# Performance work log

Measured on AMD Instinct MI355X. Metric: run time of the kernel, lower is better.

The kernel has to match this reference:

```python
import jax, jax.numpy as jnp
import numpy as np

B, Q, C = 8, 100, 1024
H, W = 64, 64
NH = 16
HD = C // NH
SCALE = HD ** -0.5
LN_EPS = 1e-5


def setup_inputs() -> dict:
    key = jax.random.key(0)
    ks = jax.random.split(key, 8)
    xav = lambda k, shp: jax.random.normal(k, shp, jnp.float32) * (2.0 / (shp[0] + shp[-1])) ** 0.5
    return {
        "tgt": jax.random.normal(ks[0], (B, Q, C), jnp.float32),
        "memory": jax.random.normal(ks[1], (B, H, W, C), jnp.float32),
        "memory_pos_emb": jax.random.normal(ks[2], (B, H, W, C), jnp.float32),
        "query_pos_emb": jax.random.normal(ks[3], (B, Q, C), jnp.float32),
        "Wq": xav(ks[4], (C, C)),
        "Wk": xav(ks[5], (C, C)),
        "Wv": xav(ks[6], (C, C)),
        "Wo": xav(ks[7], (C, C)),
        "bo": jnp.zeros((C,), jnp.float32),
        "ln_gamma": jnp.ones((C,), jnp.float32),
        "ln_beta": jnp.zeros((C,), jnp.float32),
    }


def _layernorm(x, g, b):
    mu = jnp.mean(x, axis=-1, keepdims=True)
    var = jnp.var(x, axis=-1, keepdims=True)
    return (x - mu) * jax.lax.rsqrt(var + LN_EPS) * g + b


def reference(tgt, memory, memory_pos_emb, query_pos_emb, Wq, Wk, Wv, Wo, bo, ln_gamma, ln_beta):
    # flatten spatial dims: [B,H,W,C] -> [B,K,C]
    mem = memory.reshape(B, H * W, C)
    mpos = memory_pos_emb.reshape(B, H * W, C)
    q_in = tgt + query_pos_emb          # [B,Q,C]
    k_in = mem + mpos                    # [B,K,C]
    # projections (torch Linear: x @ W.T), split heads -> [B,nh,*,hd]
    q = (q_in @ Wq.T).reshape(B, Q, NH, HD).transpose(0, 2, 1, 3)
    k = (k_in @ Wk.T).reshape(B, -1, NH, HD).transpose(0, 2, 1, 3)
    v = (mem @ Wv.T).reshape(B, -1, NH, HD).transpose(0, 2, 1, 3)
    dots = jnp.einsum('bhid,bhjd->bhij', q, k) * SCALE   # [B,nh,Q,K]
    # slot attention: softmax over QUERY axis, then renormalize over keys
    attn = jax.nn.softmax(dots, axis=2)
    attn = attn / (jnp.sum(attn, axis=-1, keepdims=True) + 1e-8)
    updates = jnp.einsum('bhij,bhjd->bhid', attn, v)     # [B,nh,Q,hd]
    updates = updates.transpose(0, 2, 1, 3).reshape(B, Q, C)
    out = updates @ Wo.T + bo
    # residual (dropout is identity in eval) + post-LayerNorm
    return _layernorm(tgt + out, ln_gamma, ln_beta)
```

## Files before the change

### kernel.cpp

```cpp
#include <hip/hip_runtime.h>

typedef unsigned short u16;
typedef __attribute__((ext_vector_type(8))) short bf16x8;
typedef __attribute__((ext_vector_type(4))) short bf16x4;
typedef __attribute__((ext_vector_type(4))) float f32x4;
typedef __attribute__((ext_vector_type(4))) unsigned short u16x4;
typedef __attribute__((ext_vector_type(4))) int i32x4;
typedef __attribute__((ext_vector_type(4))) float f4;

#define DI __device__ __forceinline__


DI u16 f2bf(float f){
  unsigned int u = __float_as_uint(f);
  return (u16)((u + 0x7FFFu + ((u >> 16) & 1u)) >> 16);
}

DI void gl_lds16(const void* g, void* l){
  __builtin_amdgcn_global_load_lds((const __attribute__((address_space(1))) unsigned int*)g,
                                   (__attribute__((address_space(3))) unsigned int*)l, 16, 0, 0);
}

__global__ __launch_bounds__(256) void prep_kv(const float* __restrict__ mem,
                                               const float* __restrict__ mpos,
                                               u16* __restrict__ kA, u16* __restrict__ vA){
  size_t gid = (size_t)blockIdx.x * 256 + threadIdx.x;
  f4 m = ((const f4*)mem)[gid];
  f4 p = ((const f4*)mpos)[gid];
  u16x4 k, v;
  #pragma unroll
  for (int j = 0; j < 4; ++j){ k[j] = f2bf(m[j] + p[j]); v[j] = f2bf(m[j]); }
  ((u16x4*)kA)[gid] = k;
  ((u16x4*)vA)[gid] = v;
}

__global__ __launch_bounds__(256) void prep_qw(const float* __restrict__ tgt,
                                               const float* __restrict__ qpos,
                                               const float* __restrict__ Wq, const float* __restrict__ Wk,
                                               const float* __restrict__ Wv, const float* __restrict__ Wo,
                                               u16* __restrict__ qA, u16* __restrict__ Wbf){
  int gid = blockIdx.x * 256 + threadIdx.x;
  const int NQ4 = 819200 / 4;
  if (gid < NQ4){
    f4 a = ((const f4*)tgt)[gid];
    f4 b = ((const f4*)qpos)[gid];
    u16x4 r;
    #pragma unroll
    for (int j = 0; j < 4; ++j) r[j] = f2bf(a[j] + b[j]);
    ((u16x4*)qA)[gid] = r;
  } else {
    int wid = gid - NQ4;
    int sel = wid >> 18;
    int off = wid & 262143;
    const float* W = (sel == 0) ? Wq : (sel == 1) ? Wk : (sel == 2) ? Wv : Wo;
    f4 w = ((const f4*)W)[off];
    u16x4 r;
    #pragma unroll
    for (int j = 0; j < 4; ++j) r[j] = f2bf(w[j]);
    ((u16x4*)(Wbf))[(size_t)sel * 262144 + off] = r;
  }
}

template<int MODE>
__global__ __launch_bounds__(256, 2) void gemm_bt(
    const u16* __restrict__ A, const u16* __restrict__ Bw,
    u16* __restrict__ Cb, float* __restrict__ Cf,
    const float* __restrict__ bias, const float* __restrict__ resid,
    int M, float scale)
{
  __shared__ u16 lA[2][128 * 32];
  __shared__ u16 lB[2][128 * 32];
  const int tid = threadIdx.x;
  const int l = tid & 63, w = tid >> 6;
  const int nwg = gridDim.x;
  int bid = blockIdx.x;
  bid = (bid & 7) * (nwg >> 3) + (bid >> 3);
  const int mb = bid >> 3, nb = bid & 7;
  const int m0 = mb * 128, n0 = nb * 128;
  const int fr = l & 15, fg = l >> 4;
  const int wr = w >> 1, wc = w & 1;

  f32x4 acc[4][4] = {};

  auto stage = [&](int buf, int kt){
    const int k0 = kt * 32;
    #pragma unroll
    for (int q = 0; q < 2; ++q){
      int r = w * 32 + q * 16 + (l >> 2);
      int ar = m0 + r; if (ar >= M) ar = M - 1;
      gl_lds16(A  + (size_t)ar * 1024 + k0 + (l & 3) * 8, &lA[buf][(w * 32 + q * 16) * 32]);
      gl_lds16(Bw + (size_t)(n0 + r) * 1024 + k0 + (l & 3) * 8, &lB[buf][(w * 32 + q * 16) * 32]);
    }
  };

  stage(0, 0);
  __syncthreads();
  for (int kt = 0; kt < 32; ++kt){
    const int cur = kt & 1;
    if (kt < 31) stage(cur ^ 1, kt + 1);
    bf16x8 av[4], bv[4];
    #pragma unroll
    for (int m = 0; m < 4; ++m)
      av[m] = *(const bf16x8*)&lA[cur][(wr * 64 + m * 16 + fr) * 32 + fg * 8];
    #pragma unroll
    for (int n = 0; n < 4; ++n)
      bv[n] = *(const bf16x8*)&lB[cur][(wc * 64 + n * 16 + fr) * 32 + fg * 8];
    #pragma unroll
    for (int m = 0; m < 4; ++m)
      #pragma unroll
      for (int n = 0; n < 4; ++n)
        acc[m][n] = __builtin_amdgcn_mfma_f32_16x16x32_bf16(av[m], bv[n], acc[m][n], 0, 0, 0);
    __syncthreads();
  }

  #pragma unroll
  for (int m = 0; m < 4; ++m){
    const int grow_base = m0 + wr * 64 + m * 16 + fg * 4;
    #pragma unroll
    for (int n = 0; n < 4; ++n){
      const int gcol = n0 + wc * 64 + n * 16 + fr;
      #pragma unroll
      for (int r = 0; r < 4; ++r){
        const int grow = grow_base + r;
        if (grow < M){
          const float v = acc[m][n][r];
          if (MODE == 0) Cb[(size_t)grow * 1024 + gcol] = f2bf(v * scale);
          else           Cf[(size_t)grow * 1024 + gcol] = v + bias[gcol] + resid[(size_t)grow * 1024 + gcol];
        }
      }
    }
  }
}

__global__ __launch_bounds__(64, 1) void attn_k(
    const u16* __restrict__ qp, const u16* __restrict__ kp, const u16* __restrict__ vp,
    float* __restrict__ updpart, float* __restrict__ rspart)
{
  const int bidx = blockIdx.x;
  const int c = bidx & 7, h = (bidx >> 3) & 15, b = bidx >> 7;
  const int bh = b * 16 + h;
  const int l = threadIdx.x;
  const int fr = l & 15, fg = l >> 4;

  __shared__ u16 qlds[112 * 64];
  for (int t = 0; t < 14; ++t){
    int chunk = t * 64 + l;
    int row = chunk >> 3, cb = chunk & 7;
    i32x4 val = {0, 0, 0, 0};
    if (row < 100)
      val = *(const i32x4*)(qp + (size_t)(b * 100 + row) * 1024 + h * 64 + cb * 8);
    *(i32x4*)((char*)qlds + row * 128 + ((cb ^ (row & 7)) * 16)) = val;
  }
  __syncthreads();

  bf16x8 qf[7][2];
  #pragma unroll
  for (int n = 0; n < 7; ++n)
    #pragma unroll
    for (int ks = 0; ks < 2; ++ks){
      int row = n * 16 + fr;
      int cb = ks * 4 + fg;
      qf[n][ks] = *(const bf16x8*)((const char*)qlds + row * 128 + ((cb ^ (row & 7)) * 16));
    }

  f32x4 acc[7][4] = {};
  float rs[7] = {};
  const f32x4 fz = {0.f, 0.f, 0.f, 0.f};
  const size_t kvbase = ((size_t)b * 4096) * 1024 + h * 64;

  for (int t = 0; t < 32; ++t){
    const int j0 = c * 512 + t * 16;
    bf16x8 kf0 = *(const bf16x8*)(kp + kvbase + (size_t)(j0 + fr) * 1024 + fg * 8);
    bf16x8 kf1 = *(const bf16x8*)(kp + kvbase + (size_t)(j0 + fr) * 1024 + 32 + fg * 8);
    f32x4 s[7];
    #pragma unroll
    for (int n = 0; n < 7; ++n){
      s[n] = __builtin_amdgcn_mfma_f32_16x16x32_bf16(kf0, qf[n][0], fz, 0, 0, 0);
      s[n] = __builtin_amdgcn_mfma_f32_16x16x32_bf16(kf1, qf[n][1], s[n], 0, 0, 0);
    }
    if (fr >= 4){ s[6][0] = -1e30f; s[6][1] = -1e30f; s[6][2] = -1e30f; s[6][3] = -1e30f; }

    float pv[7][4];
    #pragma unroll
    for (int r = 0; r < 4; ++r){
      float m = s[0][r];
      #pragma unroll
      for (int n = 1; n < 7; ++n) m = fmaxf(m, s[n][r]);
      m = fmaxf(m, __shfl_xor(m, 1)); m = fmaxf(m, __shfl_xor(m, 2));
      m = fmaxf(m, __shfl_xor(m, 4)); m = fmaxf(m, __shfl_xor(m, 8));
      float sum = 0.f;
      #pragma unroll
      for (int n = 0; n < 7; ++n){ float e = __expf(s[n][r] - m); pv[n][r] = e; sum += e; }
      sum += __shfl_xor(sum, 1); sum += __shfl_xor(sum, 2);
      sum += __shfl_xor(sum, 4); sum += __shfl_xor(sum, 8);
      float inv = 1.0f / sum;
      #pragma unroll
      for (int n = 0; n < 7; ++n) pv[n][r] *= inv;
    }

    bf16x4 pk[7];
    #pragma unroll
    for (int n = 0; n < 7; ++n){
      rs[n] += pv[n][0] + pv[n][1] + pv[n][2] + pv[n][3];
      bf16x4 t4;
      t4[0] = (short)f2bf(pv[n][0]); t4[1] = (short)f2bf(pv[n][1]);
      t4[2] = (short)f2bf(pv[n][2]); t4[3] = (short)f2bf(pv[n][3]);
      pk[n] = t4;
    }

    bf16x4 vf[4];
    #pragma unroll
    for (int dt = 0; dt < 4; ++dt){
      bf16x4 tv;
      #pragma unroll
      for (int jj = 0; jj < 4; ++jj)
        tv[jj] = (short)vp[kvbase + (size_t)(j0 + fg * 4 + jj) * 1024 + dt * 16 + fr];
      vf[dt] = tv;
    }

    #pragma unroll
    for (int n = 0; n < 7; ++n)
      #pragma unroll
      for (int dt = 0; dt < 4; ++dt)
        acc[n][dt] = __builtin_amdgcn_mfma_f32_16x16x16bf16_1k(vf[dt], pk[n], acc[n][dt], 0, 0, 0);
  }

  #pragma unroll
  for (int n = 0; n < 7; ++n){
    float v = rs[n];
    v += __shfl_xor(v, 16); v += __shfl_xor(v, 32);
    if (l < 16) rspart[((size_t)c * 128 + bh) * 112 + n * 16 + l] = v;
  }
  float* ub = updpart + ((size_t)c * 128 + bh) * 64 * 112;
  #pragma unroll
  for (int n = 0; n < 7; ++n)
    #pragma unroll
    for (int dt = 0; dt < 4; ++dt)
      #pragma unroll
      for (int r = 0; r < 4; ++r){
        int d = dt * 16 + fg * 4 + r;
        int i = n * 16 + fr;
        ub[d * 112 + i] = acc[n][dt][r];
      }
}

__global__ __launch_bounds__(256) void nrm_k(const float* __restrict__ updpart,
                                             const float* __restrict__ rspart,
                                             u16* __restrict__ updn){
  int gid = blockIdx.x * 256 + threadIdx.x;
  int b = gid / 102400;
  int rem = gid % 102400;
  int i = rem / 1024;
  int cc = rem & 1023;
  int h = cc >> 6, d = cc & 63;
  int bh = b * 16 + h;
  float sum = 0.f, rsum = 0.f;
  #pragma unroll
  for (int c = 0; c < 8; ++c){
    sum  += updpart[(((size_t)c * 128 + bh) * 64 + d) * 112 + i];
    rsum += rspart[((size_t)c * 128 + bh) * 112 + i];
  }
  updn[gid] = f2bf(sum / (rsum + 1e-8f));
}

__global__ __launch_bounds__(256) void ln_k(const float* __restrict__ x,
                                            const float* __restrict__ g,
                                            const float* __restrict__ be,
                                            float* __restrict__ out){
  const int row = blockIdx.x;
  const int tid = threadIdx.x;
  const f4 xv = *(const f4*)(x + (size_t)row * 1024 + tid * 4);
  float s = xv[0] + xv[1] + xv[2] + xv[3];
  float q = xv[0]*xv[0] + xv[1]*xv[1] + xv[2]*xv[2] + xv[3]*xv[3];
  #pragma unroll
  for (int m = 1; m < 64; m <<= 1){ s += __shfl_xor(s, m); q += __shfl_xor(q, m); }
  __shared__ float ss[4], qq[4];
  const int w = tid >> 6;
  if ((tid & 63) == 0){ ss[w] = s; qq[w] = q; }
  __syncthreads();
  s = ss[0] + ss[1] + ss[2] + ss[3];
  q = qq[0] + qq[1] + qq[2] + qq[3];
  const float mu = s * (1.0f / 1024.0f);
  const float var = q * (1.0f / 1024.0f) - mu * mu;
  const float rstd = rsqrtf(var + 1e-5f);
  const f4 gv = *(const f4*)(g + tid * 4);
  const f4 bv = *(const f4*)(be + tid * 4);
  f4 o;
  #pragma unroll
  for (int j = 0; j < 4; ++j) o[j] = (xv[j] - mu) * rstd * gv[j] + bv[j];
  *(f4*)(out + (size_t)row * 1024 + tid * 4) = o;
}

extern "C" void kernel_launch(void* const* d_in, const int* in_sizes, int n_in,
                              void* d_out, int out_size, void* d_ws, size_t ws_size,
                              hipStream_t stream)
{
  const float* tgt   = (const float*)d_in[0];
  const float* mem   = (const float*)d_in[1];
  const float* mpos  = (const float*)d_in[2];
  const float* qpos  = (const float*)d_in[3];
  const float* Wq    = (const float*)d_in[4];
  const float* Wk    = (const float*)d_in[5];
  const float* Wv    = (const float*)d_in[6];
  const float* Wo    = (const float*)d_in[7];
  const float* bo    = (const float*)d_in[8];
  const float* gamma = (const float*)d_in[9];
  const float* beta  = (const float*)d_in[10];

  char* ws = (char*)d_ws;
  u16* qA     = (u16*)(ws + 0);
  u16* Wbf    = (u16*)(ws + 1638400);
  u16* kA     = (u16*)(ws + 10027008);
  u16* vA     = (u16*)(ws + 77135872);
  u16* qproj  = (u16*)(ws + 144244736);
  u16* kproj  = (u16*)(ws + 145883136);
  u16* vproj  = kA;
  float* updpart = (float*)(ws + 77135872);
  float* rspart  = (float*)(ws + 77135872 + 29360128);
  u16*   updn    = (u16*)  (ws + 77135872 + 29818880);
  float* resid   = (float*)(ws + 77135872 + 31457280);

  prep_kv<<<32768, 256, 0, stream>>>(mem, mpos, kA, vA);
  prep_qw<<<4896, 256, 0, stream>>>(tgt, qpos, Wq, Wk, Wv, Wo, qA, Wbf);
  gemm_bt<0><<<56,   256, 0, stream>>>(qA, Wbf,            qproj, nullptr, nullptr, nullptr, 800,   0.125f);
  gemm_bt<0><<<2048, 256, 0, stream>>>(kA, Wbf + 1048576,  kproj, nullptr, nullptr, nullptr, 32768, 1.0f);
  gemm_bt<0><<<2048, 256, 0, stream>>>(vA, Wbf + 2097152,  vproj, nullptr, nullptr, nullptr, 32768, 1.0f);
  attn_k<<<1024, 64, 0, stream>>>(qproj, kproj, vproj, updpart, rspart);
  nrm_k<<<3200, 256, 0, stream>>>(updpart, rspart, updn);
  gemm_bt<1><<<56, 256, 0, stream>>>(updn, Wbf + 3145728, nullptr, resid, bo, tgt, 800, 1.0f);
  ln_k<<<800, 256, 0, stream>>>(resid, gamma, beta, (float*)d_out);
}
```

Before: 415.8 us.

## Fuse prep kernels, reorder GEMM LDS layout, pipeline attention K/V loads

Merges the two fp32-to-bf16 prep kernels into one launch, with each thread converting 8 elements per iteration using nontemporal loads. The GEMM LDS tiles are rearranged so each 16-row fragment is stored contiguously in MFMA lane order, making fragment reads linear per lane. The attention kernel prefetches the next K tile into registers and stages V through a double-buffered LDS tile instead of doing scalar strided global reads. The normalize kernel is remapped so threads walk the contiguous query index, which makes its reads of the partial sums coalesced. The cost is extra LDS and registers in the attention kernel, and wasted padding threads in the normalize kernel.

```diff
diff --git a/kernel.cpp b/kernel.cpp
--- a/kernel.cpp
+++ b/kernel.cpp
@@ -5,6 +5,7 @@
 typedef __attribute__((ext_vector_type(4))) short bf16x4;
 typedef __attribute__((ext_vector_type(4))) float f32x4;
 typedef __attribute__((ext_vector_type(4))) unsigned short u16x4;
+typedef __attribute__((ext_vector_type(8))) unsigned short u16x8;
 typedef __attribute__((ext_vector_type(4))) int i32x4;
 typedef __attribute__((ext_vector_type(4))) float f4;
 
@@ -21,43 +22,53 @@
                                    (__attribute__((address_space(3))) unsigned int*)l, 16, 0, 0);
 }
 
-__global__ __launch_bounds__(256) void prep_kv(const float* __restrict__ mem,
-                                               const float* __restrict__ mpos,
-                                               u16* __restrict__ kA, u16* __restrict__ vA){
-  size_t gid = (size_t)blockIdx.x * 256 + threadIdx.x;
-  f4 m = ((const f4*)mem)[gid];
-  f4 p = ((const f4*)mpos)[gid];
-  u16x4 k, v;
-  #pragma unroll
-  for (int j = 0; j < 4; ++j){ k[j] = f2bf(m[j] + p[j]); v[j] = f2bf(m[j]); }
-  ((u16x4*)kA)[gid] = k;
-  ((u16x4*)vA)[gid] = v;
-}
-
-__global__ __launch_bounds__(256) void prep_qw(const float* __restrict__ tgt,
-                                               const float* __restrict__ qpos,
-                                               const float* __restrict__ Wq, const float* __restrict__ Wk,
-                                               const float* __restrict__ Wv, const float* __restrict__ Wo,
-                                               u16* __restrict__ qA, u16* __restrict__ Wbf){
-  int gid = blockIdx.x * 256 + threadIdx.x;
-  const int NQ4 = 819200 / 4;
-  if (gid < NQ4){
-    f4 a = ((const f4*)tgt)[gid];
-    f4 b = ((const f4*)qpos)[gid];
-    u16x4 r;
-    #pragma unroll
-    for (int j = 0; j < 4; ++j) r[j] = f2bf(a[j] + b[j]);
-    ((u16x4*)qA)[gid] = r;
+__global__ __launch_bounds__(256) void prep_all(const float* __restrict__ mem,
+                                                const float* __restrict__ mpos,
+                                                const float* __restrict__ tgt,
+                                                const float* __restrict__ qpos,
+                                                const float* __restrict__ Wq, const float* __restrict__ Wk,
+                                                const float* __restrict__ Wv, const float* __restrict__ Wo,
+                                                u16* __restrict__ kA, u16* __restrict__ vA,
+                                                u16* __restrict__ qA, u16* __restrict__ Wbf){
+  if (blockIdx.x < 4096){
+    const int t = blockIdx.x * 256 + threadIdx.x;
+    #pragma unroll
+    for (int i = 0; i < 4; ++i){
+      const size_t g = (size_t)t + (size_t)i * 1048576;
+      f4 m0 = __builtin_nontemporal_load((const f4*)mem  + g * 2);
+      f4 m1 = __builtin_nontemporal_load((const f4*)mem  + g * 2 + 1);
+      f4 p0 = __builtin_nontemporal_load((const f4*)mpos + g * 2);
+      f4 p1 = __builtin_nontemporal_load((const f4*)mpos + g * 2 + 1);
+      u16x8 k, v;
+      #pragma unroll
+      for (int j = 0; j < 4; ++j){
+        k[j]     = f2bf(m0[j] + p0[j]);  v[j]     = f2bf(m0[j]);
+        k[j + 4] = f2bf(m1[j] + p1[j]);  v[j + 4] = f2bf(m1[j]);
+      }
+      ((u16x8*)kA)[g] = k;
+      ((u16x8*)vA)[g] = v;
+    }
   } else {
-    int wid = gid - NQ4;
-    int sel = wid >> 18;
-    int off = wid & 262143;
-    const float* W = (sel == 0) ? Wq : (sel == 1) ? Wk : (sel == 2) ? Wv : Wo;
-    f4 w = ((const f4*)W)[off];
-    u16x4 r;
-    #pragma unroll
-    for (int j = 0; j < 4; ++j) r[j] = f2bf(w[j]);
-    ((u16x4*)(Wbf))[(size_t)sel * 262144 + off] = r;
+    int gid = (blockIdx.x - 4096) * 256 + threadIdx.x;
+    const int NQ4 = 819200 / 4;
+    if (gid < NQ4){
+      f4 a = ((const f4*)tgt)[gid];
+      f4 b = ((const f4*)qpos)[gid];
+      u16x4 r;
+      #pragma unroll
+      for (int j = 0; j < 4; ++j) r[j] = f2bf(a[j] + b[j]);
+      ((u16x4*)qA)[gid] = r;
+    } else {
+      int wid = gid - NQ4;
+      int sel = wid >> 18;
+      int off = wid & 262143;
+      const float* W = (sel == 0) ? Wq : (sel == 1) ? Wk : (sel == 2) ? Wv : Wo;
+      f4 w = ((const f4*)W)[off];
+      u16x4 r;
+      #pragma unroll
+      for (int j = 0; j < 4; ++j) r[j] = f2bf(w[j]);
+      ((u16x4*)(Wbf))[(size_t)sel * 262144 + off] = r;
+    }
   }
 }
 
@@ -68,8 +79,8 @@
     const float* __restrict__ bias, const float* __restrict__ resid,
     int M, float scale)
 {
-  __shared__ u16 lA[2][128 * 32];
-  __shared__ u16 lB[2][128 * 32];
+  __shared__ __align__(16) u16 lA[2][8 * 512];
+  __shared__ __align__(16) u16 lB[2][8 * 512];
   const int tid = threadIdx.x;
   const int l = tid & 63, w = tid >> 6;
   const int nwg = gridDim.x;
@@ -83,13 +94,13 @@
   f32x4 acc[4][4] = {};
 
   auto stage = [&](int buf, int kt){
-    const int k0 = kt * 32;
+    const int k0 = kt * 32 + fg * 8;
     #pragma unroll
     for (int q = 0; q < 2; ++q){
-      int r = w * 32 + q * 16 + (l >> 2);
-      int ar = m0 + r; if (ar >= M) ar = M - 1;
-      gl_lds16(A  + (size_t)ar * 1024 + k0 + (l & 3) * 8, &lA[buf][(w * 32 + q * 16) * 32]);
-      gl_lds16(Bw + (size_t)(n0 + r) * 1024 + k0 + (l & 3) * 8, &lB[buf][(w * 32 + q * 16) * 32]);
+      const int sb = w * 2 + q;
+      int ar = m0 + sb * 16 + fr; if (ar >= M) ar = M - 1;
+      gl_lds16(A  + (size_t)ar * 1024 + k0, &lA[buf][sb * 512]);
+      gl_lds16(Bw + (size_t)(n0 + sb * 16 + fr) * 1024 + k0, &lB[buf][sb * 512]);
     }
   };
 
@@ -101,10 +112,10 @@
     bf16x8 av[4], bv[4];
     #pragma unroll
     for (int m = 0; m < 4; ++m)
-      av[m] = *(const bf16x8*)&lA[cur][(wr * 64 + m * 16 + fr) * 32 + fg * 8];
+      av[m] = *(const bf16x8*)((const char*)&lA[cur][(wr * 4 + m) * 512] + l * 16);
     #pragma unroll
     for (int n = 0; n < 4; ++n)
-      bv[n] = *(const bf16x8*)&lB[cur][(wc * 64 + n * 16 + fr) * 32 + fg * 8];
+      bv[n] = *(const bf16x8*)((const char*)&lB[cur][(wc * 4 + n) * 512] + l * 16);
     #pragma unroll
     for (int m = 0; m < 4; ++m)
       #pragma unroll
@@ -143,6 +154,8 @@
   const int fr = l & 15, fg = l >> 4;
 
   __shared__ u16 qlds[112 * 64];
+  __shared__ __align__(16) u16 vlds[2][16 * 64];
+
   for (int t = 0; t < 14; ++t){
     int chunk = t * 64 + l;
     int row = chunk >> 3, cb = chunk & 7;
@@ -167,16 +180,43 @@
   float rs[7] = {};
   const f32x4 fz = {0.f, 0.f, 0.f, 0.f};
   const size_t kvbase = ((size_t)b * 4096) * 1024 + h * 64;
+  const int j00 = c * 512;
+
+  const u16* ksrc = kp + kvbase + (size_t)fr * 1024 + fg * 8;
+  const u16* vsrc = vp + kvbase + (size_t)(l >> 3) * 1024 + (l & 7) * 8;
+
+  auto loadK = [&](int t, bf16x8& k0, bf16x8& k1){
+    const size_t ro = (size_t)(j00 + t * 16) * 1024;
+    k0 = *(const bf16x8*)(ksrc + ro);
+    k1 = *(const bf16x8*)(ksrc + ro + 32);
+  };
+  auto loadV = [&](int t, bf16x8& a, bf16x8& bb){
+    const size_t ro = (size_t)(j00 + t * 16) * 1024;
+    a  = *(const bf16x8*)(vsrc + ro);
+    bb = *(const bf16x8*)(vsrc + ro + 8 * 1024);
+  };
+  auto writeV = [&](int buf, bf16x8 a, bf16x8 bb){
+    *(bf16x8*)&vlds[buf][l * 8] = a;
+    *(bf16x8*)&vlds[buf][512 + l * 8] = bb;
+  };
+
+  bf16x8 kc0, kc1, kn0, kn1, vn0, vn1;
+  loadK(0, kc0, kc1);
+  loadV(0, vn0, vn1);
+  writeV(0, vn0, vn1);
 
   for (int t = 0; t < 32; ++t){
-    const int j0 = c * 512 + t * 16;
-    bf16x8 kf0 = *(const bf16x8*)(kp + kvbase + (size_t)(j0 + fr) * 1024 + fg * 8);
-    bf16x8 kf1 = *(const bf16x8*)(kp + kvbase + (size_t)(j0 + fr) * 1024 + 32 + fg * 8);
+    const int cur = t & 1;
+    if (t < 31){
+      loadK(t + 1, kn0, kn1);
+      loadV(t + 1, vn0, vn1);
+    }
+
     f32x4 s[7];
     #pragma unroll
     for (int n = 0; n < 7; ++n){
-      s[n] = __builtin_amdgcn_mfma_f32_16x16x32_bf16(kf0, qf[n][0], fz, 0, 0, 0);
-      s[n] = __builtin_amdgcn_mfma_f32_16x16x32_bf16(kf1, qf[n][1], s[n], 0, 0, 0);
+      s[n] = __builtin_amdgcn_mfma_f32_16x16x32_bf16(kc0, qf[n][0], fz, 0, 0, 0);
+      s[n] = __builtin_amdgcn_mfma_f32_16x16x32_bf16(kc1, qf[n][1], s[n], 0, 0, 0);
     }
     if (fr >= 4){ s[6][0] = -1e30f; s[6][1] = -1e30f; s[6][2] = -1e30f; s[6][3] = -1e30f; }
 
@@ -214,7 +254,7 @@
       bf16x4 tv;
       #pragma unroll
       for (int jj = 0; jj < 4; ++jj)
-        tv[jj] = (short)vp[kvbase + (size_t)(j0 + fg * 4 + jj) * 1024 + dt * 16 + fr];
+        tv[jj] = (short)vlds[cur][(fg * 4 + jj) * 64 + dt * 16 + fr];
       vf[dt] = tv;
     }
 
@@ -223,6 +263,11 @@
       #pragma unroll
       for (int dt = 0; dt < 4; ++dt)
         acc[n][dt] = __builtin_amdgcn_mfma_f32_16x16x16bf16_1k(vf[dt], pk[n], acc[n][dt], 0, 0, 0);
+
+    if (t < 31){
+      writeV(cur ^ 1, vn0, vn1);
+      kc0 = kn0; kc1 = kn1;
+    }
   }
 
   #pragma unroll
@@ -244,23 +289,22 @@
       }
 }
 
-__global__ __launch_bounds__(256) void nrm_k(const float* __restrict__ updpart,
+__global__ __launch_bounds__(128) void nrm_k(const float* __restrict__ updpart,
                                              const float* __restrict__ rspart,
                                              u16* __restrict__ updn){
-  int gid = blockIdx.x * 256 + threadIdx.x;
-  int b = gid / 102400;
-  int rem = gid % 102400;
-  int i = rem / 1024;
-  int cc = rem & 1023;
-  int h = cc >> 6, d = cc & 63;
-  int bh = b * 16 + h;
+  const int bid = blockIdx.x;
+  const int d = bid & 63, h = (bid >> 6) & 15, b = bid >> 10;
+  const int bh = b * 16 + h;
+  const int tid = threadIdx.x;
+  const int i = (tid < 112) ? tid : 111;
   float sum = 0.f, rsum = 0.f;
   #pragma unroll
-  for (int c = 0; c < 8; ++c){
-    sum  += updpart[(((size_t)c * 128 + bh) * 64 + d) * 112 + i];
-    rsum += rspart[((size_t)c * 128 + bh) * 112 + i];
-  }
-  updn[gid] = f2bf(sum / (rsum + 1e-8f));
+  for (int cc = 0; cc < 8; ++cc){
+    sum  += updpart[(((size_t)cc * 128 + bh) * 64 + d) * 112 + i];
+    rsum += rspart[((size_t)cc * 128 + bh) * 112 + i];
+  }
+  if (tid < 100)
+    updn[((size_t)b * 100 + tid) * 1024 + h * 64 + d] = f2bf(sum / (rsum + 1e-8f));
 }
 
 __global__ __launch_bounds__(256) void ln_k(const float* __restrict__ x,
@@ -320,13 +364,12 @@
   u16*   updn    = (u16*)  (ws + 77135872 + 29818880);
   float* resid   = (float*)(ws + 77135872 + 31457280);
 
-  prep_kv<<<32768, 256, 0, stream>>>(mem, mpos, kA, vA);
-  prep_qw<<<4896, 256, 0, stream>>>(tgt, qpos, Wq, Wk, Wv, Wo, qA, Wbf);
-  gemm_bt<0><<<56,   256, 0, stream>>>(qA, Wbf,            qproj, nullptr, nullptr, nullptr, 800,   0.125f);
-  gemm_bt<0><<<2048, 256, 0, stream>>>(kA, Wbf + 1048576,  kproj, nullptr, nullptr, nullptr, 32768, 1.0f);
-  gemm_bt<0><<<2048, 256, 0, stream>>>(vA, Wbf + 2097152,  vproj, nullptr, nullptr, nullptr, 32768, 1.0f);
+  prep_all<<<8992, 256, 0, stream>>>(mem, mpos, tgt, qpos, Wq, Wk, Wv, Wo, kA, vA, qA, Wbf);
+  gemm_bt<0><<<56,   256, 0, stream>>>(qA, Wbf, qproj, nullptr, nullptr, nullptr, 800, 0.125f);
+  gemm_bt<0><<<2048, 256, 0, stream>>>(kA, Wbf + 1048576, kproj, nullptr, nullptr, nullptr, 32768, 1.0f);
+  gemm_bt<0><<<2048, 256, 0, stream>>>(vA, Wbf + 2097152, vproj, nullptr, nullptr, nullptr, 32768, 1.0f);
   attn_k<<<1024, 64, 0, stream>>>(qproj, kproj, vproj, updpart, rspart);
-  nrm_k<<<3200, 256, 0, stream>>>(updpart, rspart, updn);
+  nrm_k<<<8192, 128, 0, stream>>>(updpart, rspart, updn);
   gemm_bt<1><<<56, 256, 0, stream>>>(updn, Wbf + 3145728, nullptr, resid, bo, tgt, 800, 1.0f);
   ln_k<<<800, 256, 0, stream>>>(resid, gamma, beta, (float*)d_out);
 }
```

Result: slower. 476.3 us (+14.6%).
